# Performance work log

Measured on AMD Instinct MI355X. Metric: run time of the kernel, lower is better.

The kernel has to match this reference:

```python
import jax, jax.numpy as jnp
import numpy as np

PI = np.pi
B, N, H, W = 32, 200000, 1024, 2048


def cloud2idx(xyz):
    # xyz: (B, N, 3) -> equirectangular grid coords in [-1, 1], shape (B, N, 2)
    theta = jnp.arctan2(jnp.linalg.norm(xyz[..., :2], axis=-1), xyz[..., 2])  # polar angle in [0, pi]
    phi = jnp.arctan2(xyz[..., 1], xyz[..., 0]) + PI                          # azimuth in [0, 2*pi]
    u = 1.0 - phi / (2.0 * PI)   # horizontal image coord in [0, 1]
    v = theta / PI               # vertical image coord in [0, 1]
    return jnp.stack([2.0 * u - 1.0, 2.0 * v - 1.0], axis=-1)


def sample_from_img(img, coord):
    # Bilinear grid_sample, align_corners=False, zeros padding.
    # img: (H, W, C); coord: (B, N, 2) in [-1, 1] (x, y order) -> (B, N, C)
    h, w = img.shape[0], img.shape[1]
    x = (coord[..., 0] + 1.0) * (w * 0.5) - 0.5
    y = (coord[..., 1] + 1.0) * (h * 0.5) - 0.5
    x0 = jnp.floor(x)
    y0 = jnp.floor(y)
    wx = x - x0
    wy = y - y0

    def gather(xi, yi):
        valid = (xi >= 0) & (xi <= w - 1) & (yi >= 0) & (yi <= h - 1)
        xc = jnp.clip(xi, 0, w - 1).astype(jnp.int32)
        yc = jnp.clip(yi, 0, h - 1).astype(jnp.int32)
        return img[yc, xc] * valid[..., None].astype(img.dtype)

    return (gather(x0, y0) * ((1.0 - wx) * (1.0 - wy))[..., None]
            + gather(x0 + 1.0, y0) * (wx * (1.0 - wy))[..., None]
            + gather(x0, y0 + 1.0) * ((1.0 - wx) * wy)[..., None]
            + gather(x0 + 1.0, y0 + 1.0) * (wx * wy)[..., None])


def setup_inputs() -> dict:
    key = jax.random.key(0)
    ks = jax.random.split(key, 7)
    return {
        "xyz": jax.random.normal(ks[0], (1, N, 3), jnp.float32) * 2.0,
        "rgb": jax.random.uniform(ks[1], (1, N, 3), jnp.float32),
        "img": jax.random.uniform(ks[2], (H, W, 3), jnp.float32),
        "translation": jax.random.normal(ks[3], (B, 3, 1), jnp.float32) * 0.1,
        "yaw": jax.random.uniform(ks[4], (B, 1), jnp.float32) * (2.0 * PI),
        "pitch": jax.random.uniform(ks[5], (B, 1), jnp.float32) * PI,
        "roll": jax.random.uniform(ks[6], (B, 1), jnp.float32) * PI,
    }


def _forward(xyz, rgb, img, translation, yaw, pitch, roll):
    z = jnp.zeros_like(yaw)
    o = jnp.ones_like(yaw)  # (B, 1)
    cr, sr = jnp.cos(roll), jnp.sin(roll)
    cp, sp = jnp.cos(pitch), jnp.sin(pitch)
    cy, sy = jnp.cos(yaw), jnp.sin(yaw)
    # (B, 3, 3) rotation matrices, same row layout as the torch code
    RX = jnp.concatenate([jnp.stack([o, z, z], -1),
                          jnp.stack([z, cr, -sr], -1),
                          jnp.stack([z, sr, cr], -1)], axis=1)
    RY = jnp.concatenate([jnp.stack([cp, z, sp], -1),
                          jnp.stack([z, o, z], -1),
                          jnp.stack([-sp, z, cp], -1)], axis=1)
    RZ = jnp.concatenate([jnp.stack([cy, -sy, z], -1),
                          jnp.stack([sy, cy, z], -1),
                          jnp.stack([z, z, o], -1)], axis=1)
    Rm = RZ @ RY @ RX  # (B, 3, 3)

    new_xyz = xyz - jnp.swapaxes(translation, 1, 2)       # (1,N,3) - (B,1,3) -> (B,N,3)
    new_xyz = jnp.einsum('bij,bnj->bni', Rm, new_xyz)      # rotate each point by row-dot

    coord = cloud2idx(new_xyz)                             # (B, N, 2)
    sample_rgb = sample_from_img(img, coord)               # (B, N, 3)

    mask = jnp.sum(sample_rgb == 0, axis=-1) != 3          # (B, N) bool
    per_pt = jnp.linalg.norm(sample_rgb - rgb, axis=-1) * mask.astype(sample_rgb.dtype)
    rgb_loss_list = per_pt.sum(-1) / mask.sum(-1).astype(per_pt.dtype)  # (B,)
    return rgb_loss_list


def reference(xyz, rgb, img, translation, yaw, pitch, roll):
    rgb_loss_list = _forward(xyz, rgb, img, translation, yaw, pitch, roll)
    return (rgb_loss_list.sum(), rgb_loss_list)
```

## Files before the change

kernel.cpp:

```cpp
#include <hip/hip_runtime.h>
#include <math.h>
#include <stdint.h>

#define PI_F 3.14159265358979323846f
#define HALF_PI_F 1.57079632679489662f

#define IMG_H 1024
#define IMG_W 2048
#define NB 8


struct __attribute__((packed, aligned(4))) U2 { uint32_t a, b; };

__device__ __forceinline__ float fast_atan2f(float y, float x) {
    float ax = fabsf(x), ay = fabsf(y);
    float mx = fmaxf(ax, ay), mn = fminf(ax, ay);
    float a = __fdividef(mn, mx);
    float s = a * a;
    float r = fmaf(s, -0.01172120f, 0.05265332f);
    r = fmaf(s, r, -0.11643287f);
    r = fmaf(s, r, 0.19354346f);
    r = fmaf(s, r, -0.33262347f);
    r = fmaf(s, r, 0.99997726f);
    r = r * a;
    if (ay > ax) r = HALF_PI_F - r;
    if (x < 0.0f) r = PI_F - r;
    return copysignf(r, y);
}

__device__ __forceinline__ uint32_t q565(float r, float g, float b) {
    uint32_t r5 = min((uint32_t)__float2uint_rn(r * 31.0f), 31u);
    uint32_t g6 = min((uint32_t)__float2uint_rn(g * 63.0f), 63u);
    uint32_t b5 = min((uint32_t)__float2uint_rn(b * 31.0f), 31u);
    return (r5 << 11) | (g6 << 5) | b5;
}

__global__ __launch_bounds__(256) void bsl_pack_setup(
        const float* __restrict__ img, uint32_t* __restrict__ vp2,
        const float* __restrict__ yaw, const float* __restrict__ pitch,
        const float* __restrict__ roll, float* __restrict__ rm,
        float* __restrict__ sums, float* __restrict__ cnts, int B) {
    if (blockIdx.x == 0 && threadIdx.x < 32) {
        int b = threadIdx.x;
        if (b < B) {
            float cr = cosf(roll[b]),  sr = sinf(roll[b]);
            float cp = cosf(pitch[b]), sp = sinf(pitch[b]);
            float cy = cosf(yaw[b]),   sy = sinf(yaw[b]);
            float RX[9] = {1.f, 0.f, 0.f,   0.f, cr, -sr,   0.f, sr,  cr};
            float RY[9] = {cp,  0.f, sp,    0.f, 1.f, 0.f,  -sp, 0.f, cp};
            float RZ[9] = {cy, -sy, 0.f,    sy,  cy, 0.f,   0.f, 0.f, 1.f};
            float A[9], M[9];
            for (int i = 0; i < 3; ++i)
                for (int j = 0; j < 3; ++j) {
                    float s = 0.f;
                    for (int k = 0; k < 3; ++k) s += RZ[i*3+k] * RY[k*3+j];
                    A[i*3+j] = s;
                }
            for (int i = 0; i < 3; ++i)
                for (int j = 0; j < 3; ++j) {
                    float s = 0.f;
                    for (int k = 0; k < 3; ++k) s += A[i*3+k] * RX[k*3+j];
                    M[i*3+j] = s;
                }
            for (int k = 0; k < 9; ++k) rm[b*9+k] = M[k];
            sums[b] = 0.f;
            cnts[b] = 0.f;
        }
    }
    int t = blockIdx.x * 256 + threadIdx.x;
    if (t < (IMG_H / 2) * (IMG_W / 4)) {
        int y2 = t >> 9;
        int xq = (t & 511) << 2;
        const float4* r0 = (const float4*)(img + ((size_t)(2 * y2) * IMG_W + xq) * 3);
        const float4* r1 = (const float4*)(img + ((size_t)(2 * y2 + 1) * IMG_W + xq) * 3);
        float4 a0 = r0[0], a1 = r0[1], a2 = r0[2];
        float4 b0 = r1[0], b1 = r1[1], b2 = r1[2];
        uint32_t lo0 = q565(a0.x, a0.y, a0.z);
        uint32_t lo1 = q565(a0.w, a1.x, a1.y);
        uint32_t lo2 = q565(a1.z, a1.w, a2.x);
        uint32_t lo3 = q565(a2.y, a2.z, a2.w);
        uint32_t hi0 = q565(b0.x, b0.y, b0.z);
        uint32_t hi1 = q565(b0.w, b1.x, b1.y);
        uint32_t hi2 = q565(b1.z, b1.w, b2.x);
        uint32_t hi3 = q565(b2.y, b2.z, b2.w);
        uint4 outv;
        outv.x = lo0 | (hi0 << 16);
        outv.y = lo1 | (hi1 << 16);
        outv.z = lo2 | (hi2 << 16);
        outv.w = lo3 | (hi3 << 16);
        *(uint4*)(vp2 + ((size_t)y2 * IMG_W + xq)) = outv;
    }
}

__global__ __launch_bounds__(256, 4) void bsl_main(
        const float* __restrict__ xyz,
        const float* __restrict__ rgb,
        const uint32_t* __restrict__ vp2,
        const float* __restrict__ trans,
        const float* __restrict__ rm,
        float* __restrict__ sums,
        float* __restrict__ cnts,
        int n_pts) {
    const int b0 = blockIdx.y * NB;
    const int tid = threadIdx.x;
    const int n = blockIdx.x * 256 + tid;

    float accs[NB], cnl[NB];
    #pragma unroll
    for (int nb = 0; nb < NB; ++nb) { accs[nb] = 0.f; cnl[nb] = 0.f; }

    if (n < n_pts) {
        float px = __builtin_nontemporal_load(&xyz[3*n+0]);
        float py = __builtin_nontemporal_load(&xyz[3*n+1]);
        float pz = __builtin_nontemporal_load(&xyz[3*n+2]);
        float r0 = __builtin_nontemporal_load(&rgb[3*n+0]);
        float r1 = __builtin_nontemporal_load(&rgb[3*n+1]);
        float r2 = __builtin_nontemporal_load(&rgb[3*n+2]);

        float xfa[NB], wxa[NB], wya[NB];
        uint32_t shp[NB];
        uint32_t pAa[NB], pAb[NB], pBa[NB], pBb[NB];
        #pragma unroll
        for (int nb = 0; nb < NB; ++nb) {
            const int b = b0 + nb;
            const float* R = rm + b * 9;
            const float* T = trans + b * 3;
            float qx = px - T[0], qy = py - T[1], qz = pz - T[2];

            float vx = R[0]*qx + R[1]*qy + R[2]*qz;
            float vy = R[3]*qx + R[4]*qy + R[5]*qz;
            float vz = R[6]*qx + R[7]*qy + R[8]*qz;

            float rxy   = sqrtf(vx*vx + vy*vy);
            float theta = fast_atan2f(rxy, vz);
            float praw  = fast_atan2f(vy, vx);

            float xf = fmaf(praw,  -325.949323452f, 1023.5f);
            float yf = fmaf(theta,  325.949323452f, -0.5f);

            float x0f = floorf(xf);
            float y0f = floorf(yf);
            xfa[nb] = xf;
            wxa[nb] = xf - x0f;
            wya[nb] = yf - y0f;

            float xbf  = fminf(fmaxf(x0f, 0.0f), 2046.0f);
            float yb0f = fminf(fmaxf(y0f,        0.0f), 1023.0f);
            float yb1f = fminf(fmaxf(y0f + 1.0f, 0.0f), 1023.0f);
            int xb  = (int)xbf;
            int y0c = (int)yb0f;
            int y1c = (int)yb1f;
            uint32_t sp = ((uint32_t)(y0c & 1) << 4) | ((uint32_t)(y1c & 1) << 12);
            if (y0f >= 0.0f)    sp |= 1u << 24;
            if (y0f <= 1022.0f) sp |= 1u << 25;
            shp[nb] = sp;

            U2 tA = *(const U2*)(vp2 + (((y0c >> 1) << 11) + xb));
            U2 tB = *(const U2*)(vp2 + (((y1c >> 1) << 11) + xb));
            pAa[nb] = tA.a; pAb[nb] = tA.b;
            pBa[nb] = tB.a; pBb[nb] = tB.b;
        }

        #pragma unroll
        for (int nb = 0; nb < NB; ++nb) {
            asm volatile("" : "+v"(pAa[nb]), "+v"(pAb[nb]),
                             "+v"(pBa[nb]), "+v"(pBb[nb]) :: "memory");
        }

        #pragma unroll
        for (int nb = 0; nb < NB; ++nb) {
            float xf = xfa[nb];
            float x0f = floorf(xf);
            float wx = wxa[nb], wy = wya[nb];

            bool vx0 = (x0f >= 0.0f);
            bool vx1 = (x0f <= 2046.0f);
            uint32_t sp = shp[nb];
            bool vy0 = (sp & (1u << 24)) != 0u;
            bool vy1 = (sp & (1u << 25)) != 0u;

            float omx = 1.0f - wx, omy = 1.0f - wy;
            float w00 = (vx0 & vy0) ? omx * omy : 0.0f;
            float w10 = (vx1 & vy0) ? wx  * omy : 0.0f;
            float w01 = (vx0 & vy1) ? omx * wy  : 0.0f;
            float w11 = (vx1 & vy1) ? wx  * wy  : 0.0f;

            uint32_t sh0 = sp & 0xffu;
            uint32_t sh1 = (sp >> 8) & 0xffu;

            bool xhi = (x0f >= 2047.0f);
            uint32_t A0 = xhi ? pAb[nb] : pAa[nb];
            uint32_t A1 = vx0 ? pAb[nb] : pAa[nb];
            uint32_t B0 = xhi ? pBb[nb] : pBa[nb];
            uint32_t B1 = vx0 ? pBb[nb] : pBa[nb];

            uint32_t t00 = (A0 >> sh0) & 0xffffu;
            uint32_t t10 = (A1 >> sh0) & 0xffffu;
            uint32_t t01 = (B0 >> sh1) & 0xffffu;
            uint32_t t11 = (B1 >> sh1) & 0xffffu;

            float r00 = (float)(t00 >> 11),        r10 = (float)(t10 >> 11);
            float r01 = (float)(t01 >> 11),        r11 = (float)(t11 >> 11);
            float g00 = (float)((t00 >> 5) & 63u), g10 = (float)((t10 >> 5) & 63u);
            float g01 = (float)((t01 >> 5) & 63u), g11 = (float)((t11 >> 5) & 63u);
            float b00 = (float)(t00 & 31u),        b10 = (float)(t10 & 31u);
            float b01 = (float)(t01 & 31u),        b11 = (float)(t11 & 31u);

            float sr = r00*w00 + r10*w10 + r01*w01 + r11*w11;
            float sg = g00*w00 + g10*w10 + g01*w01 + g11*w11;
            float sb = b00*w00 + b10*w10 + b01*w01 + b11*w11;

            bool m = !((sr == 0.0f) && (sg == 0.0f) && (sb == 0.0f));

            float d0 = fmaf(sr, 1.0f / 31.0f, -r0);
            float d1 = fmaf(sg, 1.0f / 63.0f, -r1);
            float d2 = fmaf(sb, 1.0f / 31.0f, -r2);
            float per = sqrtf(d0*d0 + d1*d1 + d2*d2);

            accs[nb] += m ? per : 0.0f;
            cnl[nb]  += m ? 1.0f : 0.0f;
        }
    }

    __shared__ float lsum[4][NB], lcnt[4][NB];
    int wid = tid >> 6;
    int lane = tid & 63;
    #pragma unroll
    for (int nb = 0; nb < NB; ++nb) {
        float a = accs[nb], c = cnl[nb];
        #pragma unroll
        for (int off = 32; off > 0; off >>= 1) {
            a += __shfl_down(a, off, 64);
            c += __shfl_down(c, off, 64);
        }
        if (lane == 0) { lsum[wid][nb] = a; lcnt[wid][nb] = c; }
    }
    __syncthreads();
    if (tid < NB * 2) {
        int nb = tid & (NB - 1);
        int k = tid >> 3;
        float v = 0.f;
        #pragma unroll
        for (int w = 0; w < 4; ++w) v += k ? lcnt[w][nb] : lsum[w][nb];
        atomicAdd(k ? &cnts[b0 + nb] : &sums[b0 + nb], v);
    }
}

__global__ void bsl_finalize(const float* __restrict__ sums,
                             const float* __restrict__ cnts,
                             float* __restrict__ out,
                             int B) {
    int b = threadIdx.x;
    float loss = 0.f;
    if (b < B) {
        loss = sums[b] / cnts[b];
        out[1 + b] = loss;
    }
    #pragma unroll
    for (int off = 32; off > 0; off >>= 1)
        loss += __shfl_down(loss, off, 64);
    if (b == 0) out[0] = loss;
}

extern "C" void kernel_launch(void* const* d_in, const int* in_sizes, int n_in,
                              void* d_out, int out_size, void* d_ws, size_t ws_size,
                              hipStream_t stream) {
    const float* xyz   = (const float*)d_in[0];
    const float* rgb   = (const float*)d_in[1];
    const float* img   = (const float*)d_in[2];
    const float* trans = (const float*)d_in[3];
    const float* yaw   = (const float*)d_in[4];
    const float* pitch = (const float*)d_in[5];
    const float* roll  = (const float*)d_in[6];
    float* out = (float*)d_out;

    const int n_pts = in_sizes[0] / 3;
    const int B     = in_sizes[3] / 3;

    float* ws   = (float*)d_ws;
    float* rm   = ws;
    float* sums = ws + 9 * B;
    float* cnts = ws + 10 * B;
    uint32_t* vp2 = (uint32_t*)((char*)d_ws + 2048);

    bsl_pack_setup<<<((IMG_H / 2) * (IMG_W / 4) + 255) / 256, 256, 0, stream>>>(
        img, vp2, yaw, pitch, roll, rm, sums, cnts, B);

    dim3 grid((n_pts + 255) / 256, B / NB);
    bsl_main<<<grid, 256, 0, stream>>>(xyz, rgb, vp2, trans, rm, sums, cnts, n_pts);

    bsl_finalize<<<1, 64, 0, stream>>>(sums, cnts, out, B);
}
```

Baseline: 148.2 us.

## Use inline-asm gathers with staged waitcnt and fuse finalize via last-block

Replaces the packed 8-byte gathers with explicit global_load_dword pairs in inline asm and adds staged s_waitcnt so the blend of early batches can start while later gathers are still in flight. Validity and shift flags are packed into one small bitfield, which removes the stored xf array and recomputed floors to cut register pressure. The separate finalize kernel is removed: a done counter reset in setup lets the last block compute the per-batch losses, saving one launch. Hand-written waitcnt inside asm volatile relies on the compiler emitting no other vector-memory ops in between, which is fragile. The nontemporal loads issued before the gathers have no explicit wait, so their completion ordering must also be checked.

```diff
diff --git a/kernel.cpp b/kernel.cpp
--- a/kernel.cpp
+++ b/kernel.cpp
@@ -9,8 +9,6 @@
 #define IMG_W 2048
 #define NB 8
 
-
-struct __attribute__((packed, aligned(4))) U2 { uint32_t a, b; };
 
 __device__ __forceinline__ float fast_atan2f(float y, float x) {
     float ax = fabsf(x), ay = fabsf(y);
@@ -39,9 +37,11 @@
         const float* __restrict__ img, uint32_t* __restrict__ vp2,
         const float* __restrict__ yaw, const float* __restrict__ pitch,
         const float* __restrict__ roll, float* __restrict__ rm,
-        float* __restrict__ sums, float* __restrict__ cnts, int B) {
+        float* __restrict__ sums, float* __restrict__ cnts,
+        unsigned* __restrict__ done, int B) {
     if (blockIdx.x == 0 && threadIdx.x < 32) {
         int b = threadIdx.x;
+        if (b == 0) *done = 0u;
         if (b < B) {
             float cr = cosf(roll[b]),  sr = sinf(roll[b]);
             float cp = cosf(pitch[b]), sp = sinf(pitch[b]);
@@ -100,7 +100,9 @@
         const float* __restrict__ rm,
         float* __restrict__ sums,
         float* __restrict__ cnts,
-        int n_pts) {
+        unsigned* __restrict__ done,
+        float* __restrict__ out,
+        int n_pts, int B) {
     const int b0 = blockIdx.y * NB;
     const int tid = threadIdx.x;
     const int n = blockIdx.x * 256 + tid;
@@ -117,7 +119,7 @@
         float r1 = __builtin_nontemporal_load(&rgb[3*n+1]);
         float r2 = __builtin_nontemporal_load(&rgb[3*n+2]);
 
-        float xfa[NB], wxa[NB], wya[NB];
+        float wxa[NB], wya[NB];
         uint32_t shp[NB];
         uint32_t pAa[NB], pAb[NB], pBa[NB], pBb[NB];
         #pragma unroll
@@ -140,7 +142,6 @@
 
             float x0f = floorf(xf);
             float y0f = floorf(yf);
-            xfa[nb] = xf;
             wxa[nb] = xf - x0f;
             wya[nb] = yf - y0f;
 
@@ -150,34 +151,49 @@
             int xb  = (int)xbf;
             int y0c = (int)yb0f;
             int y1c = (int)yb1f;
-            uint32_t sp = ((uint32_t)(y0c & 1) << 4) | ((uint32_t)(y1c & 1) << 12);
-            if (y0f >= 0.0f)    sp |= 1u << 24;
-            if (y0f <= 1022.0f) sp |= 1u << 25;
+
+            uint32_t sp = (uint32_t)(y0c & 1) | ((uint32_t)(y1c & 1) << 1);
+            if (y0f >= 0.0f)     sp |= 4u;
+            if (y0f <= 1022.0f)  sp |= 8u;
+            if (x0f >= 0.0f)     sp |= 16u;
+            if (x0f <= 2046.0f)  sp |= 32u;
+            if (x0f >= 2047.0f)  sp |= 64u;
             shp[nb] = sp;
 
-            U2 tA = *(const U2*)(vp2 + (((y0c >> 1) << 11) + xb));
-            U2 tB = *(const U2*)(vp2 + (((y1c >> 1) << 11) + xb));
-            pAa[nb] = tA.a; pAb[nb] = tA.b;
-            pBa[nb] = tB.a; pBb[nb] = tB.b;
-        }
+            const uint32_t* aA = vp2 + (((y0c >> 1) << 11) + xb);
+            const uint32_t* aB = vp2 + (((y1c >> 1) << 11) + xb);
+            uint32_t la0, la1, lb0, lb1;
+            asm volatile("global_load_dword %0, %1, off"          : "=v"(la0) : "v"(aA));
+            asm volatile("global_load_dword %0, %1, off offset:4" : "=v"(la1) : "v"(aA));
+            asm volatile("global_load_dword %0, %1, off"          : "=v"(lb0) : "v"(aB));
+            asm volatile("global_load_dword %0, %1, off offset:4" : "=v"(lb1) : "v"(aB));
+            pAa[nb] = la0; pAb[nb] = la1;
+            pBa[nb] = lb0; pBb[nb] = lb1;
+        }
+
+        asm volatile("s_waitcnt vmcnt(24)"
+            : "+v"(pAa[0]), "+v"(pAb[0]), "+v"(pBa[0]), "+v"(pBb[0]),
+              "+v"(pAa[1]), "+v"(pAb[1]), "+v"(pBa[1]), "+v"(pBb[1]));
+        asm volatile("s_waitcnt vmcnt(16)"
+            : "+v"(pAa[2]), "+v"(pAb[2]), "+v"(pBa[2]), "+v"(pBb[2]),
+              "+v"(pAa[3]), "+v"(pAb[3]), "+v"(pBa[3]), "+v"(pBb[3]));
+        asm volatile("s_waitcnt vmcnt(8)"
+            : "+v"(pAa[4]), "+v"(pAb[4]), "+v"(pBa[4]), "+v"(pBb[4]),
+              "+v"(pAa[5]), "+v"(pAb[5]), "+v"(pBa[5]), "+v"(pBb[5]));
+        asm volatile("s_waitcnt vmcnt(0)"
+            : "+v"(pAa[6]), "+v"(pAb[6]), "+v"(pBa[6]), "+v"(pBb[6]),
+              "+v"(pAa[7]), "+v"(pAb[7]), "+v"(pBa[7]), "+v"(pBb[7]));
 
         #pragma unroll
         for (int nb = 0; nb < NB; ++nb) {
-            asm volatile("" : "+v"(pAa[nb]), "+v"(pAb[nb]),
-                             "+v"(pBa[nb]), "+v"(pBb[nb]) :: "memory");
-        }
-
-        #pragma unroll
-        for (int nb = 0; nb < NB; ++nb) {
-            float xf = xfa[nb];
-            float x0f = floorf(xf);
+            uint32_t sp = shp[nb];
             float wx = wxa[nb], wy = wya[nb];
 
-            bool vx0 = (x0f >= 0.0f);
-            bool vx1 = (x0f <= 2046.0f);
-            uint32_t sp = shp[nb];
-            bool vy0 = (sp & (1u << 24)) != 0u;
-            bool vy1 = (sp & (1u << 25)) != 0u;
+            bool vy0 = (sp & 4u)  != 0u;
+            bool vy1 = (sp & 8u)  != 0u;
+            bool vx0 = (sp & 16u) != 0u;
+            bool vx1 = (sp & 32u) != 0u;
+            bool xhi = (sp & 64u) != 0u;
 
             float omx = 1.0f - wx, omy = 1.0f - wy;
             float w00 = (vx0 & vy0) ? omx * omy : 0.0f;
@@ -185,10 +201,9 @@
             float w01 = (vx0 & vy1) ? omx * wy  : 0.0f;
             float w11 = (vx1 & vy1) ? wx  * wy  : 0.0f;
 
-            uint32_t sh0 = sp & 0xffu;
-            uint32_t sh1 = (sp >> 8) & 0xffu;
-
-            bool xhi = (x0f >= 2047.0f);
+            uint32_t sh0 = (sp & 1u) << 4;
+            uint32_t sh1 = (sp & 2u) << 3;
+
             uint32_t A0 = xhi ? pAb[nb] : pAa[nb];
             uint32_t A1 = vx0 ? pAb[nb] : pAa[nb];
             uint32_t B0 = xhi ? pBb[nb] : pBa[nb];
@@ -244,22 +259,29 @@
         for (int w = 0; w < 4; ++w) v += k ? lcnt[w][nb] : lsum[w][nb];
         atomicAdd(k ? &cnts[b0 + nb] : &sums[b0 + nb], v);
     }
-}
-
-__global__ void bsl_finalize(const float* __restrict__ sums,
-                             const float* __restrict__ cnts,
-                             float* __restrict__ out,
-                             int B) {
-    int b = threadIdx.x;
-    float loss = 0.f;
-    if (b < B) {
-        loss = sums[b] / cnts[b];
-        out[1 + b] = loss;
-    }
-    #pragma unroll
-    for (int off = 32; off > 0; off >>= 1)
-        loss += __shfl_down(loss, off, 64);
-    if (b == 0) out[0] = loss;
+
+    __threadfence();
+    __shared__ bool isLast;
+    if (tid == 0) {
+        unsigned prev = atomicAdd(done, 1u);
+        isLast = (prev == gridDim.x * gridDim.y - 1u);
+    }
+    __syncthreads();
+    if (isLast && tid < 64) {
+        __threadfence();
+        int b = tid;
+        float loss = 0.f;
+        if (b < B) {
+            float s = __hip_atomic_load(&sums[b], __ATOMIC_RELAXED, __HIP_MEMORY_SCOPE_AGENT);
+            float c = __hip_atomic_load(&cnts[b], __ATOMIC_RELAXED, __HIP_MEMORY_SCOPE_AGENT);
+            loss = s / c;
+            out[1 + b] = loss;
+        }
+        #pragma unroll
+        for (int off = 32; off > 0; off >>= 1)
+            loss += __shfl_down(loss, off, 64);
+        if (b == 0) out[0] = loss;
+    }
 }
 
 extern "C" void kernel_launch(void* const* d_in, const int* in_sizes, int n_in,
@@ -281,13 +303,13 @@
     float* rm   = ws;
     float* sums = ws + 9 * B;
     float* cnts = ws + 10 * B;
+    unsigned* done = (unsigned*)(ws + 11 * B);
     uint32_t* vp2 = (uint32_t*)((char*)d_ws + 2048);
 
     bsl_pack_setup<<<((IMG_H / 2) * (IMG_W / 4) + 255) / 256, 256, 0, stream>>>(
-        img, vp2, yaw, pitch, roll, rm, sums, cnts, B);
+        img, vp2, yaw, pitch, roll, rm, sums, cnts, done, B);
 
     dim3 grid((n_pts + 255) / 256, B / NB);
-    bsl_main<<<grid, 256, 0, stream>>>(xyz, rgb, vp2, trans, rm, sums, cnts, n_pts);
-
-    bsl_finalize<<<1, 64, 0, stream>>>(sums, cnts, out, B);
-}
+    bsl_main<<<grid, 256, 0, stream>>>(xyz, rgb, vp2, trans, rm, sums, cnts,
+                                       done, out, n_pts, B);
+}
```

Result: slower. 388.5 us (+162.1%).

## Stage image rows through LDS in pack kernel and fuse finalize via last-block counter

Applied to the files above, without the earlier changes.

The pack kernel now assigns one block per pair of image rows. It copies both rows into shared memory with coalesced float4 loads, then has each thread quantize 8 consecutive pixels and write them out as two uint4 stores. The separate finalize kernel is removed: each main block increments a done counter, and the last block computes the per-batch losses and their sum. This drops one kernel launch and aims to improve load coalescing. In exchange it adds a global atomic and fences per block, and uses about 48KB of LDS per pack block, which may limit occupancy.

```diff
diff --git a/kernel.cpp b/kernel.cpp
--- a/kernel.cpp
+++ b/kernel.cpp
@@ -39,9 +39,15 @@
         const float* __restrict__ img, uint32_t* __restrict__ vp2,
         const float* __restrict__ yaw, const float* __restrict__ pitch,
         const float* __restrict__ roll, float* __restrict__ rm,
-        float* __restrict__ sums, float* __restrict__ cnts, int B) {
-    if (blockIdx.x == 0 && threadIdx.x < 32) {
-        int b = threadIdx.x;
+        float* __restrict__ sums, float* __restrict__ cnts,
+        unsigned* __restrict__ done, int B) {
+    __shared__ float lds[2][IMG_W * 3];
+    const int y2 = blockIdx.x;
+    const int tid = threadIdx.x;
+
+    if (y2 == 0 && tid < 32) {
+        int b = tid;
+        if (b == 0) *done = 0u;
         if (b < B) {
             float cr = cosf(roll[b]),  sr = sinf(roll[b]);
             float cp = cosf(pitch[b]), sp = sinf(pitch[b]);
@@ -67,29 +73,30 @@
             cnts[b] = 0.f;
         }
     }
-    int t = blockIdx.x * 256 + threadIdx.x;
-    if (t < (IMG_H / 2) * (IMG_W / 4)) {
-        int y2 = t >> 9;
-        int xq = (t & 511) << 2;
-        const float4* r0 = (const float4*)(img + ((size_t)(2 * y2) * IMG_W + xq) * 3);
-        const float4* r1 = (const float4*)(img + ((size_t)(2 * y2 + 1) * IMG_W + xq) * 3);
-        float4 a0 = r0[0], a1 = r0[1], a2 = r0[2];
-        float4 b0 = r1[0], b1 = r1[1], b2 = r1[2];
-        uint32_t lo0 = q565(a0.x, a0.y, a0.z);
-        uint32_t lo1 = q565(a0.w, a1.x, a1.y);
-        uint32_t lo2 = q565(a1.z, a1.w, a2.x);
-        uint32_t lo3 = q565(a2.y, a2.z, a2.w);
-        uint32_t hi0 = q565(b0.x, b0.y, b0.z);
-        uint32_t hi1 = q565(b0.w, b1.x, b1.y);
-        uint32_t hi2 = q565(b1.z, b1.w, b2.x);
-        uint32_t hi3 = q565(b2.y, b2.z, b2.w);
-        uint4 outv;
-        outv.x = lo0 | (hi0 << 16);
-        outv.y = lo1 | (hi1 << 16);
-        outv.z = lo2 | (hi2 << 16);
-        outv.w = lo3 | (hi3 << 16);
-        *(uint4*)(vp2 + ((size_t)y2 * IMG_W + xq)) = outv;
-    }
+
+    const float4* s0 = (const float4*)(img + (size_t)(2 * y2)     * IMG_W * 3);
+    const float4* s1 = (const float4*)(img + (size_t)(2 * y2 + 1) * IMG_W * 3);
+    float4* d0 = (float4*)lds[0];
+    float4* d1 = (float4*)lds[1];
+    #pragma unroll
+    for (int i = 0; i < 6; ++i) {
+        d0[tid + 256 * i] = s0[tid + 256 * i];
+        d1[tid + 256 * i] = s1[tid + 256 * i];
+    }
+    __syncthreads();
+
+    const int xb = tid * 8;
+    uint32_t w[8];
+    #pragma unroll
+    for (int j = 0; j < 8; ++j) {
+        int x3 = (xb + j) * 3;
+        uint32_t lo = q565(lds[0][x3], lds[0][x3+1], lds[0][x3+2]);
+        uint32_t hi = q565(lds[1][x3], lds[1][x3+1], lds[1][x3+2]);
+        w[j] = lo | (hi << 16);
+    }
+    uint4* dst = (uint4*)(vp2 + ((size_t)y2 * IMG_W + xb));
+    dst[0] = make_uint4(w[0], w[1], w[2], w[3]);
+    dst[1] = make_uint4(w[4], w[5], w[6], w[7]);
 }
 
 __global__ __launch_bounds__(256, 4) void bsl_main(
@@ -100,7 +107,9 @@
         const float* __restrict__ rm,
         float* __restrict__ sums,
         float* __restrict__ cnts,
-        int n_pts) {
+        unsigned* __restrict__ done,
+        float* __restrict__ out,
+        int n_pts, int B) {
     const int b0 = blockIdx.y * NB;
     const int tid = threadIdx.x;
     const int n = blockIdx.x * 256 + tid;
@@ -244,22 +253,29 @@
         for (int w = 0; w < 4; ++w) v += k ? lcnt[w][nb] : lsum[w][nb];
         atomicAdd(k ? &cnts[b0 + nb] : &sums[b0 + nb], v);
     }
-}
-
-__global__ void bsl_finalize(const float* __restrict__ sums,
-                             const float* __restrict__ cnts,
-                             float* __restrict__ out,
-                             int B) {
-    int b = threadIdx.x;
-    float loss = 0.f;
-    if (b < B) {
-        loss = sums[b] / cnts[b];
-        out[1 + b] = loss;
-    }
-    #pragma unroll
-    for (int off = 32; off > 0; off >>= 1)
-        loss += __shfl_down(loss, off, 64);
-    if (b == 0) out[0] = loss;
+
+    __threadfence();
+    __shared__ bool isLast;
+    if (tid == 0) {
+        unsigned prev = atomicAdd(done, 1u);
+        isLast = (prev == gridDim.x * gridDim.y - 1u);
+    }
+    __syncthreads();
+    if (isLast && tid < 64) {
+        __threadfence();
+        int b = tid;
+        float loss = 0.f;
+        if (b < B) {
+            float s = __hip_atomic_load(&sums[b], __ATOMIC_RELAXED, __HIP_MEMORY_SCOPE_AGENT);
+            float c = __hip_atomic_load(&cnts[b], __ATOMIC_RELAXED, __HIP_MEMORY_SCOPE_AGENT);
+            loss = s / c;
+            out[1 + b] = loss;
+        }
+        #pragma unroll
+        for (int off = 32; off > 0; off >>= 1)
+            loss += __shfl_down(loss, off, 64);
+        if (b == 0) out[0] = loss;
+    }
 }
 
 extern "C" void kernel_launch(void* const* d_in, const int* in_sizes, int n_in,
@@ -281,13 +297,13 @@
     float* rm   = ws;
     float* sums = ws + 9 * B;
     float* cnts = ws + 10 * B;
+    unsigned* done = (unsigned*)(ws + 11 * B);
     uint32_t* vp2 = (uint32_t*)((char*)d_ws + 2048);
 
-    bsl_pack_setup<<<((IMG_H / 2) * (IMG_W / 4) + 255) / 256, 256, 0, stream>>>(
-        img, vp2, yaw, pitch, roll, rm, sums, cnts, B);
+    bsl_pack_setup<<<IMG_H / 2, 256, 0, stream>>>(
+        img, vp2, yaw, pitch, roll, rm, sums, cnts, done, B);
 
     dim3 grid((n_pts + 255) / 256, B / NB);
-    bsl_main<<<grid, 256, 0, stream>>>(xyz, rgb, vp2, trans, rm, sums, cnts, n_pts);
-
-    bsl_finalize<<<1, 64, 0, stream>>>(sums, cnts, out, B);
-}
+    bsl_main<<<grid, 256, 0, stream>>>(xyz, rgb, vp2, trans, rm, sums, cnts,
+                                       done, out, n_pts, B);
+}
```

Result: slower. 395.1 us (+166.6%).
